# Kernel optimization log

Measured on AMD Instinct MI355X. Metric: run time of the kernel, lower is better.

Reference implementation:

```python
import jax, jax.numpy as jnp
import numpy as np

B, S, H = 2, 2048, 512
N, D = 8, 64
EPS = 1e-6


def setup_inputs() -> dict:
    key = jax.random.key(0)
    ks = jax.random.split(key, 8)
    scale = 0.02
    return {
        "query": jax.random.normal(ks[0], (B, S, H), jnp.float32),
        "key": jax.random.normal(ks[1], (B, S, H), jnp.float32),
        "value": jax.random.normal(ks[2], (B, S, H), jnp.float32),
        "wq": jax.random.normal(ks[3], (H, N, D), jnp.float32) * scale,
        "bq": jnp.zeros((N, D), jnp.float32),
        "wk": jax.random.normal(ks[4], (H, N, D), jnp.float32) * scale,
        "bk": jnp.zeros((N, D), jnp.float32),
        "wv": jax.random.normal(ks[5], (H, N, D), jnp.float32) * scale,
        "bv": jnp.zeros((N, D), jnp.float32),
        "wo": jax.random.normal(ks[6], (N, D, H), jnp.float32) * scale,
        "bo": jnp.zeros((H,), jnp.float32),
        "step": 0,
    }


def _feature_map(x):
    # elu(x) + 1 (positive feature map for linear attention)
    return jax.nn.elu(x) + 1.0


def reference(query, key, value, wq, bq, wk, bk, wv, bv, wo, bo, step):
    # QKV projections: [B,S,H] -> [B,S,N,D]
    q = jnp.einsum('bsh,hnd->bsnd', query, wq) + bq
    k = jnp.einsum('bsh,hnd->bsnd', key, wk) + bk
    v = jnp.einsum('bsh,hnd->bsnd', value, wv) + bv

    phi_q = _feature_map(q)
    phi_k = _feature_map(k)

    b, s, n, d = k.shape
    # fold batch & heads: [S, B*N, D]
    pq = phi_q.transpose(1, 0, 2, 3).reshape(s, b * n, d)
    pk = phi_k.transpose(1, 0, 2, 3).reshape(s, b * n, d)
    vv = v.transpose(1, 0, 2, 3).reshape(s, b * n, d)

    # causal linear attention via prefix sums
    # state: cumulative sum of outer products phi_k v^T -> [S, B*N, D, D]
    st = jnp.cumsum(jnp.einsum('sbh,sbd->sbhd', pk, vv), axis=0)
    qs = jnp.einsum('sbhd,sbh->sbd', st, pq)
    z = jnp.cumsum(pk, axis=0)
    qz = jnp.einsum('sbh,sbh->sb', pq, z) + EPS
    a_v = qs / qz[..., None]
    a_v = a_v.transpose(1, 0, 2).reshape(b, s, n, d)

    # output projection: [B,S,N,D] -> [B,S,H]
    return jnp.einsum('bsnd,ndh->bsh', a_v, wo) + bo
```

## Files before the change

### kernel.cpp

```cpp
#include <hip/hip_runtime.h>
#include <hip/hip_bf16.h>
#include <cstdint>

#define B_    2
#define S_    2048
#define H_    512
#define N_    8
#define D_    64
#define BS_   4096
#define CHUNK 64
#define NCH   32
#define NBN   16
#define EPS_  1e-6f

typedef __attribute__((ext_vector_type(4))) float  f32x4;
typedef __attribute__((ext_vector_type(8))) short  short8;
typedef __attribute__((ext_vector_type(4))) short  short4_t;

static __device__ __forceinline__ unsigned short f2bf(float x) {
    __hip_bfloat16 h = __float2bfloat16(x);
    return *reinterpret_cast<unsigned short*>(&h);
}
static __device__ __forceinline__ float bf2f(unsigned short u) {
    unsigned int v = ((unsigned int)u) << 16;
    float f;
    __builtin_memcpy(&f, &v, 4);
    return f;
}

__global__ __launch_bounds__(256) void convert_wt_kernel(
    const float* __restrict__ wq, const float* __restrict__ wk,
    const float* __restrict__ wv, const float* __restrict__ wo,
    unsigned short* __restrict__ wqt, unsigned short* __restrict__ wkt,
    unsigned short* __restrict__ wvt, unsigned short* __restrict__ wot)
{
    const int m = blockIdx.z;
    const float* W = (m == 0) ? wq : (m == 1) ? wk : (m == 2) ? wv : wo;
    unsigned short* Wt = (m == 0) ? wqt : (m == 1) ? wkt : (m == 2) ? wvt : wot;

    __shared__ float t[64][65];
    const int k0 = blockIdx.y * 64, c0 = blockIdx.x * 64;
    const int tid = threadIdx.x;
    const int rr = tid >> 6;
    const int cc = tid & 63;
#pragma unroll
    for (int p = 0; p < 16; p++) {
        int kl = rr + p * 4;
        t[kl][cc] = W[(size_t)(k0 + kl) * 512 + c0 + cc];
    }
    __syncthreads();
#pragma unroll
    for (int p = 0; p < 16; p++) {
        int cl = rr + p * 4;
        Wt[(size_t)(c0 + cl) * 512 + k0 + cc] = f2bf(t[cc][cl]);
    }
}

template<int MODE>
__device__ __forceinline__ void mfma_gemm_body(
    unsigned short (* __restrict__ As)[72], unsigned short (* __restrict__ Bs)[72],
    const void* __restrict__ Xv, const unsigned short* __restrict__ Wt,
    const float* __restrict__ bias,
    unsigned short* __restrict__ Obf, unsigned short* __restrict__ Ot,
    float* __restrict__ Of)
{
    const int tid  = threadIdx.x;
    const int lane = tid & 63;
    const int w    = tid >> 6;
    const int wm   = (w & 1) * 64;
    const int wn   = (w >> 1) * 32;
    const int row0 = blockIdx.y * 128;
    const int col0 = blockIdx.x * 64;
    const int frow = lane & 15;
    const int fk   = (lane >> 4) * 8;

    f32x4 acc[4][2];
#pragma unroll
    for (int m = 0; m < 4; m++)
#pragma unroll
        for (int n = 0; n < 2; n++) acc[m][n] = (f32x4){0.f, 0.f, 0.f, 0.f};

    const int lr = tid >> 3;
    const int lc = (tid & 7) * 8;

    for (int k0 = 0; k0 < 512; k0 += 64) {
#pragma unroll
        for (int p = 0; p < 4; p++) {
            int r = lr + p * 32;
            if (MODE == 3) {
                const unsigned short* X = (const unsigned short*)Xv;
                *reinterpret_cast<short8*>(&As[r][lc]) =
                    *reinterpret_cast<const short8*>(X + (size_t)(row0 + r) * 512 + k0 + lc);
            } else {
                const float* X = (const float*)Xv;
                const float* src = X + (size_t)(row0 + r) * 512 + k0 + lc;
                float4 x0 = *reinterpret_cast<const float4*>(src);
                float4 x1 = *reinterpret_cast<const float4*>(src + 4);
                short8 o;
                o[0] = (short)f2bf(x0.x); o[1] = (short)f2bf(x0.y);
                o[2] = (short)f2bf(x0.z); o[3] = (short)f2bf(x0.w);
                o[4] = (short)f2bf(x1.x); o[5] = (short)f2bf(x1.y);
                o[6] = (short)f2bf(x1.z); o[7] = (short)f2bf(x1.w);
                *reinterpret_cast<short8*>(&As[r][lc]) = o;
            }
        }
#pragma unroll
        for (int p = 0; p < 2; p++) {
            int r = (tid >> 3) + p * 32;
            *reinterpret_cast<short8*>(&Bs[r][lc]) =
                *reinterpret_cast<const short8*>(Wt + (size_t)(col0 + r) * 512 + k0 + lc);
        }
        __syncthreads();
#pragma unroll
        for (int kk = 0; kk < 64; kk += 32) {
            short8 a[4], b[2];
#pragma unroll
            for (int m = 0; m < 4; m++)
                a[m] = *reinterpret_cast<const short8*>(&As[wm + m * 16 + frow][kk + fk]);
#pragma unroll
            for (int n = 0; n < 2; n++)
                b[n] = *reinterpret_cast<const short8*>(&Bs[wn + n * 16 + frow][kk + fk]);
#pragma unroll
            for (int m = 0; m < 4; m++)
#pragma unroll
                for (int n = 0; n < 2; n++)
                    acc[m][n] = __builtin_amdgcn_mfma_f32_16x16x32_bf16(
                        a[m], b[n], acc[m][n], 0, 0, 0);
        }
        __syncthreads();
    }

#pragma unroll
    for (int n = 0; n < 2; n++) {
        int col = col0 + wn + n * 16 + frow;
        float bv_ = bias[col];
#pragma unroll
        for (int m = 0; m < 4; m++) {
            int rbase = row0 + wm + m * 16 + (lane >> 4) * 4;
            short4_t t4;
#pragma unroll
            for (int r = 0; r < 4; r++) {
                float val = acc[m][n][r] + bv_;
                if (MODE == 0 || MODE == 1)
                    val = (val > 0.f) ? (val + 1.f) : __expf(val);
                if (MODE == 3) {
                    Of[(size_t)(rbase + r) * 512 + col] = val;
                } else {
                    unsigned short ub = f2bf(val);
                    t4[r] = (short)ub;
                    if (MODE == 0 || MODE == 1)
                        Obf[(size_t)(rbase + r) * 512 + col] = ub;
                }
            }
            if (MODE == 1 || MODE == 2) {
                int bb = rbase >> 11;
                int t_ = rbase & 2047;
                *reinterpret_cast<short4_t*>(
                    Ot + (size_t)bb * (512 * 2048) + (size_t)col * 2048 + t_) = t4;
            }
        }
    }
}

__global__ __launch_bounds__(256) void qkv_proj_kernel(
    const float* __restrict__ q_in, const float* __restrict__ k_in,
    const float* __restrict__ v_in,
    const unsigned short* __restrict__ wqt, const unsigned short* __restrict__ wkt,
    const unsigned short* __restrict__ wvt,
    const float* __restrict__ bq, const float* __restrict__ bk, const float* __restrict__ bv,
    unsigned short* __restrict__ pq, unsigned short* __restrict__ pk,
    unsigned short* __restrict__ pkT, unsigned short* __restrict__ pvT)
{
    __shared__ unsigned short As[128][72];
    __shared__ unsigned short Bs[64][72];
    int m = blockIdx.z;
    if (m == 0)      mfma_gemm_body<0>(As, Bs, q_in, wqt, bq, pq, nullptr, nullptr);
    else if (m == 1) mfma_gemm_body<1>(As, Bs, k_in, wkt, bk, pk, pkT, nullptr);
    else             mfma_gemm_body<2>(As, Bs, v_in, wvt, bv, nullptr, pvT, nullptr);
}

__global__ __launch_bounds__(256) void out_proj_kernel(
    const unsigned short* __restrict__ avb, const unsigned short* __restrict__ wot,
    const float* __restrict__ bo, float* __restrict__ out)
{
    __shared__ unsigned short As[128][72];
    __shared__ unsigned short Bs[64][72];
    mfma_gemm_body<3>(As, Bs, avb, wot, bo, nullptr, nullptr, out);
}

__global__ __launch_bounds__(256) void chunk_kvscan_kernel(
    const unsigned short* __restrict__ pkT, const unsigned short* __restrict__ pvT,
    unsigned short* __restrict__ Mb, float* __restrict__ zb)
{
    __shared__ float waveTot[4][256];
    __shared__ float zTot[4][16];

    const int tile = blockIdx.x;
    const int bn   = blockIdx.y;
    const int d0   = (tile >> 2) * 16;
    const int h0   = (tile & 3) * 16;
    const int b = bn >> 3, n = bn & 7;
    const int tid = threadIdx.x, lane = tid & 63, w = tid >> 6;
    const int frow = lane & 15, grp = lane >> 4, fk = grp * 8;
    const bool do_z = (tile >> 2) == 0;

    const size_t vrow = (size_t)b * (512 * 2048) + (size_t)(n * 64 + d0 + frow) * 2048;
    const size_t krow = (size_t)b * (512 * 2048) + (size_t)(n * 64 + h0 + frow) * 2048;

    f32x4 run = (f32x4){0.f, 0.f, 0.f, 0.f};
    f32x4 loc[8];
    float runz = 0.f, locz[8];

#pragma unroll
    for (int c = 0; c < 8; c++) {
        int t0 = (w * 8 + c) * 64;
        loc[c] = run;
        locz[c] = runz;
        short8 a0 = *reinterpret_cast<const short8*>(pvT + vrow + t0 + fk);
        short8 a1 = *reinterpret_cast<const short8*>(pvT + vrow + t0 + 32 + fk);
        short8 b0 = *reinterpret_cast<const short8*>(pkT + krow + t0 + fk);
        short8 b1 = *reinterpret_cast<const short8*>(pkT + krow + t0 + 32 + fk);
        run = __builtin_amdgcn_mfma_f32_16x16x32_bf16(a0, b0, run, 0, 0, 0);
        run = __builtin_amdgcn_mfma_f32_16x16x32_bf16(a1, b1, run, 0, 0, 0);
        if (do_z) {
            float zp = 0.f;
#pragma unroll
            for (int j = 0; j < 8; j++) zp += bf2f((unsigned short)b0[j]) + bf2f((unsigned short)b1[j]);
            zp += __shfl_xor(zp, 16);
            zp += __shfl_xor(zp, 32);
            runz += zp;
        }
    }

#pragma unroll
    for (int r = 0; r < 4; r++)
        waveTot[w][(grp * 4 + r) * 16 + frow] = run[r];
    if (do_z && lane < 16) zTot[w][frow] = runz;
    __syncthreads();

    f32x4 carry = (f32x4){0.f, 0.f, 0.f, 0.f};
    float carryz = 0.f;
    for (int pw = 0; pw < w; pw++) {
#pragma unroll
        for (int r = 0; r < 4; r++)
            carry[r] += waveTot[pw][(grp * 4 + r) * 16 + frow];
        carryz += zTot[pw][frow];
    }

#pragma unroll
    for (int c = 0; c < 8; c++) {
        size_t mbase = ((size_t)bn * NCH + (w * 8 + c)) * 4096;
#pragma unroll
        for (int r = 0; r < 4; r++)
            Mb[mbase + (size_t)(d0 + grp * 4 + r) * 64 + h0 + frow] = f2bf(carry[r] + loc[c][r]);
        if (do_z && lane < 16)
            zb[((size_t)bn * NCH + (w * 8 + c)) * 64 + h0 + frow] = carryz + locz[c];
    }
}

__global__ __launch_bounds__(256) void chunk_attn_kernel(
    const unsigned short* __restrict__ pq, const unsigned short* __restrict__ pk,
    const unsigned short* __restrict__ pvT, const unsigned short* __restrict__ Mb,
    const float* __restrict__ zb, unsigned short* __restrict__ av)
{
    __shared__ unsigned short Qs[64][72], Ks[64][72], VT[64][72], Ab[64][72];
    __shared__ float zs[64], dqz4[64][4], dAS[64];

    const int c = blockIdx.x, bn = blockIdx.y;
    const int b = bn >> 3, n = bn & 7;
    const int row0 = b * S_ + c * 64;
    const int col0 = n * 64;
    const int t0 = c * 64;
    const size_t vbase = (size_t)b * 512 * 2048;
    const size_t mbase = ((size_t)bn * NCH + c) * 4096;
    const int tid = threadIdx.x, lane = tid & 63, w = tid >> 6;

#pragma unroll
    for (int p = 0; p < 2; p++) {
        int r  = (tid >> 3) + p * 32;
        int c8 = (tid & 7) * 8;
        *reinterpret_cast<short8*>(&Qs[r][c8]) =
            *reinterpret_cast<const short8*>(pq + (size_t)(row0 + r) * 512 + col0 + c8);
        *reinterpret_cast<short8*>(&Ks[r][c8]) =
            *reinterpret_cast<const short8*>(pk + (size_t)(row0 + r) * 512 + col0 + c8);
        *reinterpret_cast<short8*>(&VT[r][c8]) =
            *reinterpret_cast<const short8*>(pvT + vbase + (size_t)(col0 + r) * 2048 + t0 + c8);
    }
    if (tid < 64) zs[tid] = zb[((size_t)bn * NCH + c) * 64 + tid];
    __syncthreads();

    const int frow = lane & 15, grp = lane >> 4, fk = grp * 8;
    const int srow = w * 16;

    f32x4 a1[4];
#pragma unroll
    for (int tf = 0; tf < 4; tf++) a1[tf] = (f32x4){0.f, 0.f, 0.f, 0.f};
#pragma unroll
    for (int ks = 0; ks < 2; ks++) {
        short8 qa = *reinterpret_cast<const short8*>(&Qs[srow + frow][ks * 32 + fk]);
#pragma unroll
        for (int tf = 0; tf < 4; tf++) {
            short8 kb = *reinterpret_cast<const short8*>(&Ks[tf * 16 + frow][ks * 32 + fk]);
            a1[tf] = __builtin_amdgcn_mfma_f32_16x16x32_bf16(qa, kb, a1[tf], 0, 0, 0);
        }
    }

    float rs[4] = {0.f, 0.f, 0.f, 0.f};
#pragma unroll
    for (int tf = 0; tf < 4; tf++) {
        int t_ = tf * 16 + frow;
#pragma unroll
        for (int r = 0; r < 4; r++) {
            int s_ = srow + grp * 4 + r;
            float v = (t_ <= s_) ? a1[tf][r] : 0.f;
            rs[r] += v;
            Ab[s_][t_] = f2bf(v);
        }
    }
#pragma unroll
    for (int msk = 1; msk < 16; msk <<= 1)
#pragma unroll
        for (int r = 0; r < 4; r++) rs[r] += __shfl_xor(rs[r], msk);
    if (frow == 0) {
#pragma unroll
        for (int r = 0; r < 4; r++) dAS[srow + grp * 4 + r] = rs[r];
    }

    {
        int s = tid & 63, part = tid >> 6;
        float sdq = 0.f;
#pragma unroll
        for (int j = 0; j < 16; j++) {
            int h = part * 16 + j;
            sdq += bf2f(Qs[s][h]) * zs[h];
        }
        dqz4[s][part] = sdq;
    }
    __syncthreads();

    f32x4 o[4];
#pragma unroll
    for (int df = 0; df < 4; df++) o[df] = (f32x4){0.f, 0.f, 0.f, 0.f};
#pragma unroll
    for (int ks = 0; ks < 2; ks++) {
        short8 aa = *reinterpret_cast<const short8*>(&Ab[srow + frow][ks * 32 + fk]);
        short8 qa = *reinterpret_cast<const short8*>(&Qs[srow + frow][ks * 32 + fk]);
#pragma unroll
        for (int df = 0; df < 4; df++) {
            short8 vb = *reinterpret_cast<const short8*>(&VT[df * 16 + frow][ks * 32 + fk]);
            short8 sp = *reinterpret_cast<const short8*>(
                Mb + mbase + (size_t)(df * 16 + frow) * 64 + ks * 32 + fk);
            o[df] = __builtin_amdgcn_mfma_f32_16x16x32_bf16(aa, vb, o[df], 0, 0, 0);
            o[df] = __builtin_amdgcn_mfma_f32_16x16x32_bf16(qa, sp, o[df], 0, 0, 0);
        }
    }

    float inv[4];
    size_t obase[4];
#pragma unroll
    for (int r = 0; r < 4; r++) {
        int s_loc = srow + grp * 4 + r;
        float dq = dqz4[s_loc][0] + dqz4[s_loc][1] + dqz4[s_loc][2] + dqz4[s_loc][3];
        inv[r] = 1.f / (dq + dAS[s_loc] + EPS_);
        int s_b = c * 64 + s_loc;
        int jj  = n * S_ + s_b;
        obase[r] = (size_t)(b * S_ + (jj >> 3)) * 512 + (size_t)(jj & 7) * 64;
    }
#pragma unroll
    for (int df = 0; df < 4; df++) {
        int d = df * 16 + frow;
#pragma unroll
        for (int r = 0; r < 4; r++)
            av[obase[r] + d] = f2bf(o[df][r] * inv[r]);
    }
}

extern "C" void kernel_launch(void* const* d_in, const int* in_sizes, int n_in,
                              void* d_out, int out_size, void* d_ws, size_t ws_size,
                              hipStream_t stream)
{
    const float* q_in = (const float*)d_in[0];
    const float* k_in = (const float*)d_in[1];
    const float* v_in = (const float*)d_in[2];
    const float* wq   = (const float*)d_in[3];
    const float* bq   = (const float*)d_in[4];
    const float* wk   = (const float*)d_in[5];
    const float* bk   = (const float*)d_in[6];
    const float* wv   = (const float*)d_in[7];
    const float* bv   = (const float*)d_in[8];
    const float* wo   = (const float*)d_in[9];
    const float* bo   = (const float*)d_in[10];
    float* out = (float*)d_out;

    const size_t PLANE = (size_t)BS_ * 512;

    float* ws = (float*)d_ws;
    float* zbuf = ws;
    unsigned short* u16 = (unsigned short*)(zbuf + 32768);
    unsigned short* Mb  = u16;
    unsigned short* pq  = Mb  + PLANE;
    unsigned short* pk  = pq  + PLANE;
    unsigned short* pkT = pk  + PLANE;
    unsigned short* pvT = pkT + PLANE;
    unsigned short* avb = pvT + PLANE;
    unsigned short* wqt = avb + PLANE;
    unsigned short* wkt = wqt + 262144;
    unsigned short* wvt = wkt + 262144;
    unsigned short* wot = wvt + 262144;

    convert_wt_kernel<<<dim3(8, 8, 4), 256, 0, stream>>>(wq, wk, wv, wo, wqt, wkt, wvt, wot);
    qkv_proj_kernel<<<dim3(8, 32, 3), 256, 0, stream>>>(
        q_in, k_in, v_in, wqt, wkt, wvt, bq, bk, bv, pq, pk, pkT, pvT);
    chunk_kvscan_kernel<<<dim3(16, NBN), 256, 0, stream>>>(pkT, pvT, Mb, zbuf);
    chunk_attn_kernel<<<dim3(NCH, NBN), 256, 0, stream>>>(pq, pk, pvT, Mb, zbuf, avb);
    out_proj_kernel<<<dim3(8, 32), 256, 0, stream>>>(avb, wot, bo, out);
}
```

Baseline: 149.0 us.

## Retile QKV and output GEMMs, prefetch state, stage attention output in LDS

The QKV projection moves to 128x128 tiles, each wave computing a 64x64 sub-tile, which halves the block count and increases reuse of the fp32 input conversion. The output projection becomes a dedicated 64x64-tile kernel with more blocks to fill the CUs. In the chunk attention kernel, the prefix-state fragments are loaded from global memory up front, one barrier moves later, and the attention output is staged through shared memory so it is written with coalesced 16-byte stores. Costs are higher register pressure in the QKV GEMM (a 4x4 accumulator array) and an extra barrier in the attention epilogue.

```diff
diff --git a/kernel.cpp b/kernel.cpp
--- a/kernel.cpp
+++ b/kernel.cpp
@@ -62,23 +62,21 @@
     const void* __restrict__ Xv, const unsigned short* __restrict__ Wt,
     const float* __restrict__ bias,
     unsigned short* __restrict__ Obf, unsigned short* __restrict__ Ot,
-    float* __restrict__ Of)
+    int row0, int col0)
 {
     const int tid  = threadIdx.x;
     const int lane = tid & 63;
     const int w    = tid >> 6;
     const int wm   = (w & 1) * 64;
-    const int wn   = (w >> 1) * 32;
-    const int row0 = blockIdx.y * 128;
-    const int col0 = blockIdx.x * 64;
+    const int wn   = (w >> 1) * 64;
     const int frow = lane & 15;
     const int fk   = (lane >> 4) * 8;
 
-    f32x4 acc[4][2];
+    f32x4 acc[4][4];
 #pragma unroll
     for (int m = 0; m < 4; m++)
 #pragma unroll
-        for (int n = 0; n < 2; n++) acc[m][n] = (f32x4){0.f, 0.f, 0.f, 0.f};
+        for (int n = 0; n < 4; n++) acc[m][n] = (f32x4){0.f, 0.f, 0.f, 0.f};
 
     const int lr = tid >> 3;
     const int lc = (tid & 7) * 8;
@@ -87,25 +85,19 @@
 #pragma unroll
         for (int p = 0; p < 4; p++) {
             int r = lr + p * 32;
-            if (MODE == 3) {
-                const unsigned short* X = (const unsigned short*)Xv;
-                *reinterpret_cast<short8*>(&As[r][lc]) =
-                    *reinterpret_cast<const short8*>(X + (size_t)(row0 + r) * 512 + k0 + lc);
-            } else {
-                const float* X = (const float*)Xv;
-                const float* src = X + (size_t)(row0 + r) * 512 + k0 + lc;
-                float4 x0 = *reinterpret_cast<const float4*>(src);
-                float4 x1 = *reinterpret_cast<const float4*>(src + 4);
-                short8 o;
-                o[0] = (short)f2bf(x0.x); o[1] = (short)f2bf(x0.y);
-                o[2] = (short)f2bf(x0.z); o[3] = (short)f2bf(x0.w);
-                o[4] = (short)f2bf(x1.x); o[5] = (short)f2bf(x1.y);
-                o[6] = (short)f2bf(x1.z); o[7] = (short)f2bf(x1.w);
-                *reinterpret_cast<short8*>(&As[r][lc]) = o;
-            }
-        }
-#pragma unroll
-        for (int p = 0; p < 2; p++) {
+            const float* X = (const float*)Xv;
+            const float* src = X + (size_t)(row0 + r) * 512 + k0 + lc;
+            float4 x0 = *reinterpret_cast<const float4*>(src);
+            float4 x1 = *reinterpret_cast<const float4*>(src + 4);
+            short8 o;
+            o[0] = (short)f2bf(x0.x); o[1] = (short)f2bf(x0.y);
+            o[2] = (short)f2bf(x0.z); o[3] = (short)f2bf(x0.w);
+            o[4] = (short)f2bf(x1.x); o[5] = (short)f2bf(x1.y);
+            o[6] = (short)f2bf(x1.z); o[7] = (short)f2bf(x1.w);
+            *reinterpret_cast<short8*>(&As[r][lc]) = o;
+        }
+#pragma unroll
+        for (int p = 0; p < 4; p++) {
             int r = (tid >> 3) + p * 32;
             *reinterpret_cast<short8*>(&Bs[r][lc]) =
                 *reinterpret_cast<const short8*>(Wt + (size_t)(col0 + r) * 512 + k0 + lc);
@@ -113,17 +105,17 @@
         __syncthreads();
 #pragma unroll
         for (int kk = 0; kk < 64; kk += 32) {
-            short8 a[4], b[2];
+            short8 a[4], b[4];
 #pragma unroll
             for (int m = 0; m < 4; m++)
                 a[m] = *reinterpret_cast<const short8*>(&As[wm + m * 16 + frow][kk + fk]);
 #pragma unroll
-            for (int n = 0; n < 2; n++)
+            for (int n = 0; n < 4; n++)
                 b[n] = *reinterpret_cast<const short8*>(&Bs[wn + n * 16 + frow][kk + fk]);
 #pragma unroll
             for (int m = 0; m < 4; m++)
 #pragma unroll
-                for (int n = 0; n < 2; n++)
+                for (int n = 0; n < 4; n++)
                     acc[m][n] = __builtin_amdgcn_mfma_f32_16x16x32_bf16(
                         a[m], b[n], acc[m][n], 0, 0, 0);
         }
@@ -131,7 +123,7 @@
     }
 
 #pragma unroll
-    for (int n = 0; n < 2; n++) {
+    for (int n = 0; n < 4; n++) {
         int col = col0 + wn + n * 16 + frow;
         float bv_ = bias[col];
 #pragma unroll
@@ -143,14 +135,10 @@
                 float val = acc[m][n][r] + bv_;
                 if (MODE == 0 || MODE == 1)
                     val = (val > 0.f) ? (val + 1.f) : __expf(val);
-                if (MODE == 3) {
-                    Of[(size_t)(rbase + r) * 512 + col] = val;
-                } else {
-                    unsigned short ub = f2bf(val);
-                    t4[r] = (short)ub;
-                    if (MODE == 0 || MODE == 1)
-                        Obf[(size_t)(rbase + r) * 512 + col] = ub;
-                }
+                unsigned short ub = f2bf(val);
+                t4[r] = (short)ub;
+                if (MODE == 0 || MODE == 1)
+                    Obf[(size_t)(rbase + r) * 512 + col] = ub;
             }
             if (MODE == 1 || MODE == 2) {
                 int bb = rbase >> 11;
@@ -172,20 +160,77 @@
     unsigned short* __restrict__ pkT, unsigned short* __restrict__ pvT)
 {
     __shared__ unsigned short As[128][72];
-    __shared__ unsigned short Bs[64][72];
+    __shared__ unsigned short Bs[128][72];
+    const int row0 = blockIdx.x * 128;
+    const int col0 = blockIdx.y * 128;
     int m = blockIdx.z;
-    if (m == 0)      mfma_gemm_body<0>(As, Bs, q_in, wqt, bq, pq, nullptr, nullptr);
-    else if (m == 1) mfma_gemm_body<1>(As, Bs, k_in, wkt, bk, pk, pkT, nullptr);
-    else             mfma_gemm_body<2>(As, Bs, v_in, wvt, bv, nullptr, pvT, nullptr);
+    if (m == 0)      mfma_gemm_body<0>(As, Bs, q_in, wqt, bq, pq, nullptr, row0, col0);
+    else if (m == 1) mfma_gemm_body<1>(As, Bs, k_in, wkt, bk, pk, pkT, row0, col0);
+    else             mfma_gemm_body<2>(As, Bs, v_in, wvt, bv, nullptr, pvT, row0, col0);
 }
 
 __global__ __launch_bounds__(256) void out_proj_kernel(
     const unsigned short* __restrict__ avb, const unsigned short* __restrict__ wot,
     const float* __restrict__ bo, float* __restrict__ out)
 {
-    __shared__ unsigned short As[128][72];
+    __shared__ unsigned short As[64][72];
     __shared__ unsigned short Bs[64][72];
-    mfma_gemm_body<3>(As, Bs, avb, wot, bo, nullptr, nullptr, out);
+    const int row0 = blockIdx.x * 64;
+    const int col0 = blockIdx.y * 64;
+    const int tid = threadIdx.x, lane = tid & 63, w = tid >> 6;
+    const int wm = (w & 1) * 32, wn = (w >> 1) * 32;
+    const int frow = lane & 15, fk = (lane >> 4) * 8;
+
+    f32x4 acc[2][2];
+#pragma unroll
+    for (int m = 0; m < 2; m++)
+#pragma unroll
+        for (int n = 0; n < 2; n++) acc[m][n] = (f32x4){0.f, 0.f, 0.f, 0.f};
+
+    const int lr = tid >> 3;
+    const int lc = (tid & 7) * 8;
+
+    for (int k0 = 0; k0 < 512; k0 += 64) {
+#pragma unroll
+        for (int p = 0; p < 2; p++) {
+            int r = lr + p * 32;
+            *reinterpret_cast<short8*>(&As[r][lc]) =
+                *reinterpret_cast<const short8*>(avb + (size_t)(row0 + r) * 512 + k0 + lc);
+            *reinterpret_cast<short8*>(&Bs[r][lc]) =
+                *reinterpret_cast<const short8*>(wot + (size_t)(col0 + r) * 512 + k0 + lc);
+        }
+        __syncthreads();
+#pragma unroll
+        for (int kk = 0; kk < 64; kk += 32) {
+            short8 a[2], b[2];
+#pragma unroll
+            for (int m = 0; m < 2; m++)
+                a[m] = *reinterpret_cast<const short8*>(&As[wm + m * 16 + frow][kk + fk]);
+#pragma unroll
+            for (int n = 0; n < 2; n++)
+                b[n] = *reinterpret_cast<const short8*>(&Bs[wn + n * 16 + frow][kk + fk]);
+#pragma unroll
+            for (int m = 0; m < 2; m++)
+#pragma unroll
+                for (int n = 0; n < 2; n++)
+                    acc[m][n] = __builtin_amdgcn_mfma_f32_16x16x32_bf16(
+                        a[m], b[n], acc[m][n], 0, 0, 0);
+        }
+        __syncthreads();
+    }
+
+#pragma unroll
+    for (int n = 0; n < 2; n++) {
+        int col = col0 + wn + n * 16 + frow;
+        float bv_ = bo[col];
+#pragma unroll
+        for (int m = 0; m < 2; m++) {
+            int rbase = row0 + wm + m * 16 + (lane >> 4) * 4;
+#pragma unroll
+            for (int r = 0; r < 4; r++)
+                out[(size_t)(rbase + r) * 512 + col] = acc[m][n][r] + bv_;
+        }
+    }
 }
 
 __global__ __launch_bounds__(256) void chunk_kvscan_kernel(
@@ -265,6 +310,7 @@
 {
     __shared__ unsigned short Qs[64][72], Ks[64][72], VT[64][72], Ab[64][72];
     __shared__ float zs[64], dqz4[64][4], dAS[64];
+    unsigned short (* __restrict__ av8)[520] = (unsigned short(*)[520])Ab;
 
     const int c = blockIdx.x, bn = blockIdx.y;
     const int b = bn >> 3, n = bn & 7;
@@ -292,6 +338,14 @@
     const int frow = lane & 15, grp = lane >> 4, fk = grp * 8;
     const int srow = w * 16;
 
+    short8 sp[2][4];
+#pragma unroll
+    for (int ks = 0; ks < 2; ks++)
+#pragma unroll
+        for (int df = 0; df < 4; df++)
+            sp[ks][df] = *reinterpret_cast<const short8*>(
+                Mb + mbase + (size_t)(df * 16 + frow) * 64 + ks * 32 + fk);
+
     f32x4 a1[4];
 #pragma unroll
     for (int tf = 0; tf < 4; tf++) a1[tf] = (f32x4){0.f, 0.f, 0.f, 0.f};
@@ -336,7 +390,6 @@
         }
         dqz4[s][part] = sdq;
     }
-    __syncthreads();
 
     f32x4 o[4];
 #pragma unroll
@@ -348,30 +401,39 @@
 #pragma unroll
         for (int df = 0; df < 4; df++) {
             short8 vb = *reinterpret_cast<const short8*>(&VT[df * 16 + frow][ks * 32 + fk]);
-            short8 sp = *reinterpret_cast<const short8*>(
-                Mb + mbase + (size_t)(df * 16 + frow) * 64 + ks * 32 + fk);
             o[df] = __builtin_amdgcn_mfma_f32_16x16x32_bf16(aa, vb, o[df], 0, 0, 0);
-            o[df] = __builtin_amdgcn_mfma_f32_16x16x32_bf16(qa, sp, o[df], 0, 0, 0);
-        }
-    }
+            o[df] = __builtin_amdgcn_mfma_f32_16x16x32_bf16(qa, sp[ks][df], o[df], 0, 0, 0);
+        }
+    }
+
+    __syncthreads();
 
     float inv[4];
-    size_t obase[4];
 #pragma unroll
     for (int r = 0; r < 4; r++) {
         int s_loc = srow + grp * 4 + r;
         float dq = dqz4[s_loc][0] + dqz4[s_loc][1] + dqz4[s_loc][2] + dqz4[s_loc][3];
         inv[r] = 1.f / (dq + dAS[s_loc] + EPS_);
-        int s_b = c * 64 + s_loc;
-        int jj  = n * S_ + s_b;
-        obase[r] = (size_t)(b * S_ + (jj >> 3)) * 512 + (size_t)(jj & 7) * 64;
     }
 #pragma unroll
     for (int df = 0; df < 4; df++) {
         int d = df * 16 + frow;
 #pragma unroll
-        for (int r = 0; r < 4; r++)
-            av[obase[r] + d] = f2bf(o[df][r] * inv[r]);
+        for (int r = 0; r < 4; r++) {
+            int s_loc = srow + grp * 4 + r;
+            av8[s_loc >> 3][(s_loc & 7) * 64 + d] = f2bf(o[df][r] * inv[r]);
+        }
+    }
+    __syncthreads();
+
+    const int orow0 = b * S_ + n * 256 + c * 8;
+#pragma unroll
+    for (int p = 0; p < 2; p++) {
+        int idx = (p * 256 + tid) * 8;
+        int rr = idx >> 9;
+        int cc = idx & 511;
+        *reinterpret_cast<short8*>(av + (size_t)(orow0 + rr) * 512 + cc) =
+            *reinterpret_cast<const short8*>(&av8[rr][cc]);
     }
 }
 
@@ -409,9 +471,9 @@
     unsigned short* wot = wvt + 262144;
 
     convert_wt_kernel<<<dim3(8, 8, 4), 256, 0, stream>>>(wq, wk, wv, wo, wqt, wkt, wvt, wot);
-    qkv_proj_kernel<<<dim3(8, 32, 3), 256, 0, stream>>>(
+    qkv_proj_kernel<<<dim3(32, 4, 3), 256, 0, stream>>>(
         q_in, k_in, v_in, wqt, wkt, wvt, bq, bk, bv, pq, pk, pkT, pvT);
     chunk_kvscan_kernel<<<dim3(16, NBN), 256, 0, stream>>>(pkT, pvT, Mb, zbuf);
     chunk_attn_kernel<<<dim3(NCH, NBN), 256, 0, stream>>>(pq, pk, pvT, Mb, zbuf, avb);
-    out_proj_kernel<<<dim3(8, 32), 256, 0, stream>>>(avb, wot, bo, out);
-}
+    out_proj_kernel<<<dim3(64, 8), 256, 0, stream>>>(avb, wot, bo, out);
+}
```

After: 140.6 us. 1.06x faster.
